# Kernel tuning notes

Measured on AMD Instinct MI355X. Metric: run time of the kernel, lower is better.

## Reference

```python
import jax, jax.numpy as jnp
import numpy as np

N = 100000        # total nodes across the batch of graphs
E = 1600000       # directed edges (avg degree 16)
B = 64            # number of graphs
IN_C = 4
HID = 128


def gcn_conv(x, W, b, src, dst, n):
    """PyG GCNConv: add self-loops, symmetric deg normalization, scatter-add."""
    h = x @ W                                   # [n, out]
    loop = jnp.arange(n)
    s = jnp.concatenate([src, loop])            # [E+n] sources (with self-loops)
    d = jnp.concatenate([dst, loop])            # [E+n] targets
    deg = jax.ops.segment_sum(jnp.ones_like(s, dtype=h.dtype), d, num_segments=n)
    dinv = jnp.where(deg > 0, jax.lax.rsqrt(deg), 0.0)
    norm = dinv[s] * dinv[d]                    # [E+n]
    out = jax.ops.segment_sum(h[s] * norm[:, None], d, num_segments=n)
    return out + b


def setup_inputs() -> dict:
    key = jax.random.key(0)
    k1, k2, k3, k4, k5, k6, k7 = jax.random.split(key, 7)
    x = jax.random.normal(k1, (N, IN_C), dtype=jnp.float32)
    edge_index = jax.random.randint(k2, (2, E), 0, N, dtype=jnp.int64)
    batch = jnp.sort(jax.random.randint(k3, (N,), 0, B, dtype=jnp.int64))
    W1 = jax.random.normal(k4, (IN_C, HID), dtype=jnp.float32) / np.sqrt(IN_C)
    b1 = jnp.zeros((HID,), dtype=jnp.float32)
    W2 = jax.random.normal(k5, (HID, HID), dtype=jnp.float32) / np.sqrt(HID)
    b2 = jnp.zeros((HID,), dtype=jnp.float32)
    return {"x": x, "edge_index": edge_index, "batch": batch,
            "W1": W1, "b1": b1, "W2": W2, "b2": b2}


def reference(x, edge_index, batch, W1, b1, W2, b2):
    src, dst = edge_index[0], edge_index[1]
    n = x.shape[0]
    h = jax.nn.relu(gcn_conv(x, W1, b1, src, dst, n))
    h = jax.nn.relu(gcn_conv(h, W2, b2, src, dst, n))
    # global_mean_pool: scatter-mean by graph id
    s = jax.ops.segment_sum(h, batch, num_segments=B)                       # [B, HID]
    cnt = jax.ops.segment_sum(jnp.ones((n,), h.dtype), batch, num_segments=B)
    return s / jnp.maximum(cnt, 1.0)[:, None]
```

## Files before the change

kernel.cpp:

```cpp
#include <hip/hip_runtime.h>

#define TPB 256
#define HID 128
#define IN_C 4
#define SLOT_C 32
#define NB 512
#define EPT 8
#define ECAP 4096
#define OVF_CAP 131072

typedef __attribute__((ext_vector_type(8))) short bf16x8;
typedef __attribute__((ext_vector_type(4))) float f32x4;

union FragU { uint4 u; bf16x8 b; };

__device__ __forceinline__ unsigned f2bf(float f) {
    unsigned u = __float_as_uint(f);
    return (u + 0x7fffu + ((u >> 16) & 1u)) >> 16;
}
__device__ __forceinline__ float bf_lo(unsigned u) { return __uint_as_float(u << 16); }
__device__ __forceinline__ float bf_hi(unsigned u) { return __uint_as_float(u & 0xffff0000u); }

__global__ void k_prep(int* cursor, float* out, int n, int outsz,
                       const float* __restrict__ W2, unsigned short* w2f,
                       const int* __restrict__ batch, float* rcnt, int bg,
                       int* ovf_cnt, int* pcur) {
    int nbA = (n + TPB - 1) / TPB;
    int b = blockIdx.x;
    if (b < nbA) {
        int i = b * TPB + threadIdx.x;
        if (i < n) cursor[i] = 0;
        if (i < outsz) out[i] = 0.0f;
    } else if (b < nbA + 64) {
        int i = (b - nbA) * TPB + threadIdx.x;
        if (i < HID * HID) {
            int j = i & 7, frag = i >> 3;
            int lane = frag & 63, blk = frag >> 6;
            int kk = blk >> 3, nt = blk & 7;
            int quad = lane >> 4, nloc = lane & 15;
            int k = kk * 32 + quad * 8 + j;
            int c = nt * 16 + nloc;
            w2f[i] = (unsigned short)f2bf(W2[k * HID + c]);
        }
    } else {
        int g = threadIdx.x;
        if (g == 0) *ovf_cnt = 0;
        for (int z = g; z < NB; z += TPB) pcur[z] = 0;
        if (g < bg) {
            int lo0 = 0, hi0 = n;
            while (lo0 < hi0) { int m = (lo0 + hi0) >> 1; if (batch[m] < g) lo0 = m + 1; else hi0 = m; }
            int lo1 = lo0, hi1 = n;
            while (lo1 < hi1) { int m = (lo1 + hi1) >> 1; if (batch[m] < g + 1) lo1 = m + 1; else hi1 = m; }
            int c = lo1 - lo0;
            rcnt[g] = 1.0f / (float)(c > 1 ? c : 1);
        }
    }
}

__global__ __launch_bounds__(256) void k_part(
        const int* __restrict__ src, const int* __restrict__ dst,
        int2* elist, int* pcur, int e, int n) {
    __shared__ int lcnt[2][NB];
    __shared__ int lbase[NB];
    int t = threadIdx.x;
    int c = (t >> 5) & 1;
    for (int z = t; z < NB; z += 256) { lcnt[0][z] = 0; lcnt[1][z] = 0; }
    __syncthreads();

    int base_i = blockIdx.x * (256 * EPT);
    int s[EPT], d[EPT], pr[EPT];
#pragma unroll
    for (int k = 0; k < EPT; k++) {
        int i = base_i + k * 256 + t;
        if (i < e) {
            s[k] = src[i];
            d[k] = dst[i];
            int p = (int)(((long long)d[k] * NB) / n);
            int r = atomicAdd(&lcnt[c][p], 1);
            pr[k] = p | (r << 9);
        } else {
            pr[k] = -1;
        }
    }
    __syncthreads();

    for (int z = t; z < NB; z += 256) {
        int tot = lcnt[0][z] + lcnt[1][z];
        lbase[z] = tot ? atomicAdd(&pcur[z], tot) : 0;
    }
    __syncthreads();

#pragma unroll
    for (int k = 0; k < EPT; k++) {
        if (pr[k] >= 0) {
            int p = pr[k] & (NB - 1);
            int r = pr[k] >> 9;
            int idx = lbase[p] + (c ? lcnt[0][p] : 0) + r;
            if (idx < ECAP)
                elist[(size_t)p * ECAP + idx] = make_int2(s[k], d[k]);
        }
    }
}

__global__ __launch_bounds__(256) void k_build(
        const int2* __restrict__ elist, const int* __restrict__ pcur,
        int* cursor, float* dinv, int* slots, int* ovf, int* ovf_cnt, int n) {
    __shared__ int lcur[512];
    int p = blockIdx.x;
    int t = threadIdx.x;
    int nlo = (int)(((long long)p * n + NB - 1) / NB);
    int nhi = (int)(((long long)(p + 1) * n + NB - 1) / NB);
    int nn = nhi - nlo;
    for (int z = t; z < nn; z += 256) lcur[z] = 0;
    __syncthreads();

    int ne = pcur[p];
    if (ne > ECAP) ne = ECAP;
    for (int j = t; j < ne; j += 256) {
        int2 ed = elist[(size_t)p * ECAP + j];
        int pos = atomicAdd(&lcur[ed.y - nlo], 1);
        if (pos < SLOT_C) {
            slots[ed.y * SLOT_C + pos] = ed.x;
        } else {
            int o = atomicAdd(ovf_cnt, 1);
            if (o < OVF_CAP) {
                ovf[2 * o] = ed.x;
                ovf[2 * o + 1] = ed.y;
            }
        }
    }
    __syncthreads();
    for (int z = t; z < nn; z += 256) {
        int dg = lcur[z];
        cursor[nlo + z] = dg;
        dinv[nlo + z] = rsqrtf((float)dg + 1.0f);
    }
}

__global__ __launch_bounds__(256) void k_g1f1(
        const int* __restrict__ cursor, const int* __restrict__ slots,
        const int* __restrict__ ovf, const int* __restrict__ ovf_cnt,
        const float* __restrict__ dinv, const float* __restrict__ x,
        const float* __restrict__ W1, const float* __restrict__ b1,
        unsigned* f1p, int n) {
    __shared__ float xs[256 * 5];
    int t = threadIdx.x;
    int v0 = blockIdx.x * 256;

    int v = v0 + t;
    if (v < n) {
        float dv = dinv[v];
        const float4* x4 = (const float4*)x;
        float4 xv = x4[v];
        float sl = dv * dv;
        float4 A = make_float4(sl * xv.x, sl * xv.y, sl * xv.z, sl * xv.w);
        float4 B = make_float4(0.f, 0.f, 0.f, 0.f);
        float4 C = make_float4(0.f, 0.f, 0.f, 0.f);
        float4 D = make_float4(0.f, 0.f, 0.f, 0.f);
        int deg = cursor[v];
        int m = deg < SLOT_C ? deg : SLOT_C;
        const int* sb = slots + v * SLOT_C;
        int e = 0;
        for (; e + 4 <= m; e += 4) {
            int s0 = sb[e], s1 = sb[e + 1], s2 = sb[e + 2], s3 = sb[e + 3];
            float n0 = dinv[s0] * dv, n1 = dinv[s1] * dv;
            float n2 = dinv[s2] * dv, n3 = dinv[s3] * dv;
            float4 r0 = x4[s0], r1 = x4[s1], r2 = x4[s2], r3 = x4[s3];
            A.x = fmaf(n0, r0.x, A.x); A.y = fmaf(n0, r0.y, A.y);
            A.z = fmaf(n0, r0.z, A.z); A.w = fmaf(n0, r0.w, A.w);
            B.x = fmaf(n1, r1.x, B.x); B.y = fmaf(n1, r1.y, B.y);
            B.z = fmaf(n1, r1.z, B.z); B.w = fmaf(n1, r1.w, B.w);
            C.x = fmaf(n2, r2.x, C.x); C.y = fmaf(n2, r2.y, C.y);
            C.z = fmaf(n2, r2.z, C.z); C.w = fmaf(n2, r2.w, C.w);
            D.x = fmaf(n3, r3.x, D.x); D.y = fmaf(n3, r3.y, D.y);
            D.z = fmaf(n3, r3.z, D.z); D.w = fmaf(n3, r3.w, D.w);
        }
        for (; e < m; e++) {
            int s = sb[e];
            float nm = dinv[s] * dv;
            float4 r = x4[s];
            A.x = fmaf(nm, r.x, A.x); A.y = fmaf(nm, r.y, A.y);
            A.z = fmaf(nm, r.z, A.z); A.w = fmaf(nm, r.w, A.w);
        }
        if (deg > SLOT_C) {
            int oc = *ovf_cnt;
            for (int k = 0; k < oc; k++) {
                if (ovf[2 * k + 1] == v) {
                    int s = ovf[2 * k];
                    float nm = dinv[s] * dv;
                    float4 r = x4[s];
                    A.x = fmaf(nm, r.x, A.x); A.y = fmaf(nm, r.y, A.y);
                    A.z = fmaf(nm, r.z, A.z); A.w = fmaf(nm, r.w, A.w);
                }
            }
        }
        xs[t * 5 + 0] = (A.x + B.x) + (C.x + D.x);
        xs[t * 5 + 1] = (A.y + B.y) + (C.y + D.y);
        xs[t * 5 + 2] = (A.z + B.z) + (C.z + D.z);
        xs[t * 5 + 3] = (A.w + B.w) + (C.w + D.w);
    }
    __syncthreads();

    int cp = t & 63;
    int c0 = cp * 2, c1 = c0 + 1;
    float w00 = W1[c0],           w01 = W1[c1];
    float w10 = W1[HID + c0],     w11 = W1[HID + c1];
    float w20 = W1[2 * HID + c0], w21 = W1[2 * HID + c1];
    float w30 = W1[3 * HID + c0], w31 = W1[3 * HID + c1];
    float bb0 = b1[c0],           bb1 = b1[c1];
    int g = t >> 6;
    for (int iter = 0; iter < 64; iter++) {
        int node = iter * 4 + g;
        int vv = v0 + node;
        if (vv >= n) break;
        float x0 = xs[node * 5 + 0], x1 = xs[node * 5 + 1];
        float x2 = xs[node * 5 + 2], x3 = xs[node * 5 + 3];
        float s0 = fmaf(x0, w00, fmaf(x1, w10, fmaf(x2, w20, fmaf(x3, w30, bb0))));
        float s1 = fmaf(x0, w01, fmaf(x1, w11, fmaf(x2, w21, fmaf(x3, w31, bb1))));
        s0 = s0 > 0.0f ? s0 : 0.0f;
        s1 = s1 > 0.0f ? s1 : 0.0f;
        f1p[(size_t)vv * 64 + cp] = f2bf(s0) | (f2bf(s1) << 16);
    }
}

__global__ __launch_bounds__(128) void k_gather2(
        const int* __restrict__ cursor, const int* __restrict__ slots,
        const int* __restrict__ ovf, const int* __restrict__ ovf_cnt,
        const float* __restrict__ dinv, const unsigned* __restrict__ f1p,
        unsigned* acc2b, int n) {
    int wv = threadIdx.x >> 6;
    int ln = threadIdx.x & 63;
    int h  = ln >> 5;
    int q  = ln & 31;
    int v = blockIdx.x * 2 + wv;
    if (v >= n) return;
    float dv = dinv[v];
    const uint2* F = (const uint2*)f1p;

    uint2 us = F[(size_t)v * 32 + q];
    float sl = (h == 0) ? dv * dv : 0.0f;
    float A[4] = { sl * bf_lo(us.x), sl * bf_hi(us.x),
                   sl * bf_lo(us.y), sl * bf_hi(us.y) };
    float B[4] = {0.f, 0.f, 0.f, 0.f};
    float C[4] = {0.f, 0.f, 0.f, 0.f};
    float D[4] = {0.f, 0.f, 0.f, 0.f};

    int deg = cursor[v];
    int m = deg < SLOT_C ? deg : SLOT_C;
    const int* sb = slots + v * SLOT_C;
    int e = 0;
    for (; e + 8 <= m; e += 8) {
        int sA = sb[e + h];
        int sB = sb[e + 2 + h];
        int sC = sb[e + 4 + h];
        int sD = sb[e + 6 + h];
        float nA = dinv[sA] * dv, nB = dinv[sB] * dv;
        float nC = dinv[sC] * dv, nD = dinv[sD] * dv;
        uint2 uA = F[(size_t)sA * 32 + q];
        uint2 uB = F[(size_t)sB * 32 + q];
        uint2 uC = F[(size_t)sC * 32 + q];
        uint2 uD = F[(size_t)sD * 32 + q];
        A[0] = fmaf(nA, bf_lo(uA.x), A[0]); A[1] = fmaf(nA, bf_hi(uA.x), A[1]);
        A[2] = fmaf(nA, bf_lo(uA.y), A[2]); A[3] = fmaf(nA, bf_hi(uA.y), A[3]);
        B[0] = fmaf(nB, bf_lo(uB.x), B[0]); B[1] = fmaf(nB, bf_hi(uB.x), B[1]);
        B[2] = fmaf(nB, bf_lo(uB.y), B[2]); B[3] = fmaf(nB, bf_hi(uB.y), B[3]);
        C[0] = fmaf(nC, bf_lo(uC.x), C[0]); C[1] = fmaf(nC, bf_hi(uC.x), C[1]);
        C[2] = fmaf(nC, bf_lo(uC.y), C[2]); C[3] = fmaf(nC, bf_hi(uC.y), C[3]);
        D[0] = fmaf(nD, bf_lo(uD.x), D[0]); D[1] = fmaf(nD, bf_hi(uD.x), D[1]);
        D[2] = fmaf(nD, bf_lo(uD.y), D[2]); D[3] = fmaf(nD, bf_hi(uD.y), D[3]);
    }
    for (; e + 2 <= m; e += 2) {
        int s = sb[e + h];
        float nm = dinv[s] * dv;
        uint2 u = F[(size_t)s * 32 + q];
        A[0] = fmaf(nm, bf_lo(u.x), A[0]); A[1] = fmaf(nm, bf_hi(u.x), A[1]);
        A[2] = fmaf(nm, bf_lo(u.y), A[2]); A[3] = fmaf(nm, bf_hi(u.y), A[3]);
    }
    if (e < m) {
        int s = sb[e];
        float nm = (h == 0) ? dinv[s] * dv : 0.0f;
        uint2 u = F[(size_t)s * 32 + q];
        A[0] = fmaf(nm, bf_lo(u.x), A[0]); A[1] = fmaf(nm, bf_hi(u.x), A[1]);
        A[2] = fmaf(nm, bf_lo(u.y), A[2]); A[3] = fmaf(nm, bf_hi(u.y), A[3]);
    }
    if (deg > SLOT_C) {
        int oc = *ovf_cnt;
        for (int k = 0; k < oc; k++) {
            if (ovf[2 * k + 1] == v && h == 0) {
                int s = ovf[2 * k];
                float nm = dinv[s] * dv;
                uint2 u = F[(size_t)s * 32 + q];
                A[0] = fmaf(nm, bf_lo(u.x), A[0]); A[1] = fmaf(nm, bf_hi(u.x), A[1]);
                A[2] = fmaf(nm, bf_lo(u.y), A[2]); A[3] = fmaf(nm, bf_hi(u.y), A[3]);
            }
        }
    }

    float o0 = (A[0] + B[0]) + (C[0] + D[0]);
    float o1 = (A[1] + B[1]) + (C[1] + D[1]);
    float o2 = (A[2] + B[2]) + (C[2] + D[2]);
    float o3 = (A[3] + B[3]) + (C[3] + D[3]);
    o0 += __shfl_xor(o0, 32, 64);
    o1 += __shfl_xor(o1, 32, 64);
    o2 += __shfl_xor(o2, 32, 64);
    o3 += __shfl_xor(o3, 32, 64);
    if (h == 0) {
        uint2 w;
        w.x = f2bf(o0) | (f2bf(o1) << 16);
        w.y = f2bf(o2) | (f2bf(o3) << 16);
        ((uint2*)acc2b)[(size_t)v * 32 + q] = w;
    }
}

__global__ __launch_bounds__(256) void k_mm2_pool(
        const unsigned* __restrict__ acc2b, const unsigned short* __restrict__ w2f,
        const float* __restrict__ b2, const int* __restrict__ batch,
        const float* __restrict__ rcnt, float* out, int n) {
    __shared__ int bch[64];
    int t = threadIdx.x;
    int w = t >> 6, lane = t & 63;
    int quad = lane >> 4, nloc = lane & 15;
    int v0 = blockIdx.x * 64;
    if (t < 64) {
        int v = v0 + t;
        bch[t] = (v < n) ? batch[v] : -1;
    }
    __syncthreads();

    int va = v0 + w * 16 + nloc;
    if (va >= n) va = n - 1;

    const uint4* A4 = (const uint4*)acc2b;
    const uint4* B4 = (const uint4*)w2f;

    f32x4 acc[8];
#pragma unroll
    for (int nt = 0; nt < 8; nt++) acc[nt] = (f32x4){0.f, 0.f, 0.f, 0.f};

#pragma unroll
    for (int kk = 0; kk < 4; kk++) {
        FragU af;
        af.u = A4[(size_t)va * 16 + kk * 4 + quad];
#pragma unroll
        for (int nt = 0; nt < 8; nt++) {
            FragU bf;
            bf.u = B4[(kk * 8 + nt) * 64 + lane];
            acc[nt] = __builtin_amdgcn_mfma_f32_16x16x32_bf16(af.b, bf.b, acc[nt], 0, 0, 0);
        }
    }

    int b0 = bch[w * 16], b15 = bch[w * 16 + 15];
    if (b0 == b15 && b0 >= 0) {
        float rc = rcnt[b0];
#pragma unroll
        for (int nt = 0; nt < 8; nt++) {
            float bias = b2[nt * 16 + nloc];
            float s = 0.f;
#pragma unroll
            for (int reg = 0; reg < 4; reg++) {
                float f = acc[nt][reg] + bias;
                s += f > 0.f ? f : 0.f;
            }
            s += __shfl_xor(s, 16, 64);
            s += __shfl_xor(s, 32, 64);
            if (lane < 16) atomicAdd(&out[b0 * HID + nt * 16 + lane], s * rc);
        }
    } else {
#pragma unroll
        for (int nt = 0; nt < 8; nt++) {
            float bias = b2[nt * 16 + nloc];
            int cur = -1; float run = 0.f;
#pragma unroll
            for (int reg = 0; reg < 4; reg++) {
                int b = bch[w * 16 + quad * 4 + reg];
                if (b < 0) continue;
                float f = acc[nt][reg] + bias;
                f = f > 0.f ? f : 0.f;
                if (b != cur) {
                    if (cur >= 0) atomicAdd(&out[cur * HID + nt * 16 + nloc], run * rcnt[cur]);
                    run = 0.f; cur = b;
                }
                run += f;
            }
            if (cur >= 0) atomicAdd(&out[cur * HID + nt * 16 + nloc], run * rcnt[cur]);
        }
    }
}

extern "C" void kernel_launch(void* const* d_in, const int* in_sizes, int n_in,
                              void* d_out, int out_size, void* d_ws, size_t ws_size,
                              hipStream_t stream) {
    const float* x   = (const float*)d_in[0];
    const int* ei    = (const int*)d_in[1];
    const int* batch = (const int*)d_in[2];
    const float* W1  = (const float*)d_in[3];
    const float* b1  = (const float*)d_in[4];
    const float* W2  = (const float*)d_in[5];
    const float* b2  = (const float*)d_in[6];
    float* out = (float*)d_out;

    int n  = in_sizes[0] / IN_C;
    int e  = in_sizes[1] / 2;
    int bg = out_size / HID;
    const int* src = ei;
    const int* dst = ei + e;

    size_t off_b = 0;
    char* base = (char*)d_ws;
    auto carve = [&](size_t bytes) -> void* {
        void* p = base + off_b;
        off_b += (bytes + 255) & ~(size_t)255;
        return p;
    };
    int*            cursor  = (int*)carve((size_t)n * 4);
    int*            slots   = (int*)carve((size_t)n * SLOT_C * 4);
    int*            ovf     = (int*)carve((size_t)OVF_CAP * 2 * 4);
    int*            ovf_cnt = (int*)carve(256);
    int*            pcur    = (int*)carve((size_t)NB * 4);
    int2*           elist   = (int2*)carve((size_t)NB * ECAP * 8);
    float*          dinv    = (float*)carve((size_t)n * 4);
    unsigned*       f1p     = (unsigned*)carve((size_t)n * 64 * 4);
    unsigned*       acc2b   = (unsigned*)carve((size_t)n * 64 * 4);
    unsigned short* w2f     = (unsigned short*)carve((size_t)HID * HID * 2);
    float*          rcnt    = (float*)carve((size_t)bg * 4);
    (void)ws_size;

    int gN = (n + TPB - 1) / TPB;
    int gP = (e + 256 * EPT - 1) / (256 * EPT);

    k_prep<<<gN + 64 + 1, TPB, 0, stream>>>(cursor, out, n, out_size, W2, w2f,
                                            batch, rcnt, bg, ovf_cnt, pcur);
    k_part<<<gP, TPB, 0, stream>>>(src, dst, elist, pcur, e, n);
    k_build<<<NB, TPB, 0, stream>>>(elist, pcur, cursor, dinv, slots, ovf, ovf_cnt, n);
    k_g1f1<<<gN, TPB, 0, stream>>>(cursor, slots, ovf, ovf_cnt, dinv, x, W1, b1, f1p, n);
    k_gather2<<<(n + 1) / 2, 128, 0, stream>>>(cursor, slots, ovf, ovf_cnt, dinv, f1p, acc2b, n);
    k_mm2_pool<<<(n + 63) / 64, 256, 0, stream>>>(acc2b, w2f, b2, batch, rcnt, out, n);
}
```

Baseline: 248.0 us.

## Fuse layer-2 gather with MFMA matmul and pooling via shared-memory rows

Merges the layer-2 neighbor gather kernel into the matmul+pool kernel. Each 256-thread block gathers 64 node rows, with each wave handling 16 nodes in turn, and stages the aggregated bf16 rows in LDS, padded to 68 words per row. It then feeds them to the MFMA tile directly. This removes the acc2b global round trip (write then read of n*128 bf16) and one kernel launch. The cost is less parallelism in the gather: 64 nodes per block processed serially per wave instead of 2 nodes per 128-thread block, which may hurt latency hiding for the random gathers.

Result: slower. 285.5 us (+15.1%).

```diff
diff --git a/kernel.cpp b/kernel.cpp
--- a/kernel.cpp
+++ b/kernel.cpp
@@ -223,114 +223,112 @@
     }
 }
 
-__global__ __launch_bounds__(128) void k_gather2(
+__global__ __launch_bounds__(256) void k_g2mm(
         const int* __restrict__ cursor, const int* __restrict__ slots,
         const int* __restrict__ ovf, const int* __restrict__ ovf_cnt,
         const float* __restrict__ dinv, const unsigned* __restrict__ f1p,
-        unsigned* acc2b, int n) {
-    int wv = threadIdx.x >> 6;
-    int ln = threadIdx.x & 63;
-    int h  = ln >> 5;
-    int q  = ln & 31;
-    int v = blockIdx.x * 2 + wv;
-    if (v >= n) return;
-    float dv = dinv[v];
-    const uint2* F = (const uint2*)f1p;
-
-    uint2 us = F[(size_t)v * 32 + q];
-    float sl = (h == 0) ? dv * dv : 0.0f;
-    float A[4] = { sl * bf_lo(us.x), sl * bf_hi(us.x),
-                   sl * bf_lo(us.y), sl * bf_hi(us.y) };
-    float B[4] = {0.f, 0.f, 0.f, 0.f};
-    float C[4] = {0.f, 0.f, 0.f, 0.f};
-    float D[4] = {0.f, 0.f, 0.f, 0.f};
-
-    int deg = cursor[v];
-    int m = deg < SLOT_C ? deg : SLOT_C;
-    const int* sb = slots + v * SLOT_C;
-    int e = 0;
-    for (; e + 8 <= m; e += 8) {
-        int sA = sb[e + h];
-        int sB = sb[e + 2 + h];
-        int sC = sb[e + 4 + h];
-        int sD = sb[e + 6 + h];
-        float nA = dinv[sA] * dv, nB = dinv[sB] * dv;
-        float nC = dinv[sC] * dv, nD = dinv[sD] * dv;
-        uint2 uA = F[(size_t)sA * 32 + q];
-        uint2 uB = F[(size_t)sB * 32 + q];
-        uint2 uC = F[(size_t)sC * 32 + q];
-        uint2 uD = F[(size_t)sD * 32 + q];
-        A[0] = fmaf(nA, bf_lo(uA.x), A[0]); A[1] = fmaf(nA, bf_hi(uA.x), A[1]);
-        A[2] = fmaf(nA, bf_lo(uA.y), A[2]); A[3] = fmaf(nA, bf_hi(uA.y), A[3]);
-        B[0] = fmaf(nB, bf_lo(uB.x), B[0]); B[1] = fmaf(nB, bf_hi(uB.x), B[1]);
-        B[2] = fmaf(nB, bf_lo(uB.y), B[2]); B[3] = fmaf(nB, bf_hi(uB.y), B[3]);
-        C[0] = fmaf(nC, bf_lo(uC.x), C[0]); C[1] = fmaf(nC, bf_hi(uC.x), C[1]);
-        C[2] = fmaf(nC, bf_lo(uC.y), C[2]); C[3] = fmaf(nC, bf_hi(uC.y), C[3]);
-        D[0] = fmaf(nD, bf_lo(uD.x), D[0]); D[1] = fmaf(nD, bf_hi(uD.x), D[1]);
-        D[2] = fmaf(nD, bf_lo(uD.y), D[2]); D[3] = fmaf(nD, bf_hi(uD.y), D[3]);
-    }
-    for (; e + 2 <= m; e += 2) {
-        int s = sb[e + h];
-        float nm = dinv[s] * dv;
-        uint2 u = F[(size_t)s * 32 + q];
-        A[0] = fmaf(nm, bf_lo(u.x), A[0]); A[1] = fmaf(nm, bf_hi(u.x), A[1]);
-        A[2] = fmaf(nm, bf_lo(u.y), A[2]); A[3] = fmaf(nm, bf_hi(u.y), A[3]);
-    }
-    if (e < m) {
-        int s = sb[e];
-        float nm = (h == 0) ? dinv[s] * dv : 0.0f;
-        uint2 u = F[(size_t)s * 32 + q];
-        A[0] = fmaf(nm, bf_lo(u.x), A[0]); A[1] = fmaf(nm, bf_hi(u.x), A[1]);
-        A[2] = fmaf(nm, bf_lo(u.y), A[2]); A[3] = fmaf(nm, bf_hi(u.y), A[3]);
-    }
-    if (deg > SLOT_C) {
-        int oc = *ovf_cnt;
-        for (int k = 0; k < oc; k++) {
-            if (ovf[2 * k + 1] == v && h == 0) {
-                int s = ovf[2 * k];
-                float nm = dinv[s] * dv;
-                uint2 u = F[(size_t)s * 32 + q];
-                A[0] = fmaf(nm, bf_lo(u.x), A[0]); A[1] = fmaf(nm, bf_hi(u.x), A[1]);
-                A[2] = fmaf(nm, bf_lo(u.y), A[2]); A[3] = fmaf(nm, bf_hi(u.y), A[3]);
-            }
-        }
-    }
-
-    float o0 = (A[0] + B[0]) + (C[0] + D[0]);
-    float o1 = (A[1] + B[1]) + (C[1] + D[1]);
-    float o2 = (A[2] + B[2]) + (C[2] + D[2]);
-    float o3 = (A[3] + B[3]) + (C[3] + D[3]);
-    o0 += __shfl_xor(o0, 32, 64);
-    o1 += __shfl_xor(o1, 32, 64);
-    o2 += __shfl_xor(o2, 32, 64);
-    o3 += __shfl_xor(o3, 32, 64);
-    if (h == 0) {
-        uint2 w;
-        w.x = f2bf(o0) | (f2bf(o1) << 16);
-        w.y = f2bf(o2) | (f2bf(o3) << 16);
-        ((uint2*)acc2b)[(size_t)v * 32 + q] = w;
-    }
-}
-
-__global__ __launch_bounds__(256) void k_mm2_pool(
-        const unsigned* __restrict__ acc2b, const unsigned short* __restrict__ w2f,
-        const float* __restrict__ b2, const int* __restrict__ batch,
-        const float* __restrict__ rcnt, float* out, int n) {
+        const unsigned short* __restrict__ w2f, const float* __restrict__ b2,
+        const int* __restrict__ batch, const float* __restrict__ rcnt,
+        float* out, int n) {
+    __shared__ unsigned arow[64][68];
     __shared__ int bch[64];
     int t = threadIdx.x;
-    int w = t >> 6, lane = t & 63;
-    int quad = lane >> 4, nloc = lane & 15;
+    int w = t >> 6, ln = t & 63;
     int v0 = blockIdx.x * 64;
     if (t < 64) {
         int v = v0 + t;
         bch[t] = (v < n) ? batch[v] : -1;
     }
-    __syncthreads();
-
-    int va = v0 + w * 16 + nloc;
-    if (va >= n) va = n - 1;
-
-    const uint4* A4 = (const uint4*)acc2b;
+    if (v0 + 64 > n) {
+        for (int z = t; z < 64 * 68; z += 256) ((unsigned*)arow)[z] = 0;
+    }
+    __syncthreads();
+
+    int h = ln >> 5;
+    int q = ln & 31;
+    const uint2* F = (const uint2*)f1p;
+    for (int nd = 0; nd < 16; nd++) {
+        int row = w * 16 + nd;
+        int v = v0 + row;
+        if (v >= n) break;
+        float dv = dinv[v];
+
+        uint2 us = F[(size_t)v * 32 + q];
+        float sl = (h == 0) ? dv * dv : 0.0f;
+        float A[4] = { sl * bf_lo(us.x), sl * bf_hi(us.x),
+                       sl * bf_lo(us.y), sl * bf_hi(us.y) };
+        float B[4] = {0.f, 0.f, 0.f, 0.f};
+        float C[4] = {0.f, 0.f, 0.f, 0.f};
+        float D[4] = {0.f, 0.f, 0.f, 0.f};
+
+        int deg = cursor[v];
+        int m = deg < SLOT_C ? deg : SLOT_C;
+        const int* sb = slots + v * SLOT_C;
+        int e = 0;
+        for (; e + 8 <= m; e += 8) {
+            int sA = sb[e + h];
+            int sB = sb[e + 2 + h];
+            int sC = sb[e + 4 + h];
+            int sD = sb[e + 6 + h];
+            float nA = dinv[sA] * dv, nB = dinv[sB] * dv;
+            float nC = dinv[sC] * dv, nD = dinv[sD] * dv;
+            uint2 uA = F[(size_t)sA * 32 + q];
+            uint2 uB = F[(size_t)sB * 32 + q];
+            uint2 uC = F[(size_t)sC * 32 + q];
+            uint2 uD = F[(size_t)sD * 32 + q];
+            A[0] = fmaf(nA, bf_lo(uA.x), A[0]); A[1] = fmaf(nA, bf_hi(uA.x), A[1]);
+            A[2] = fmaf(nA, bf_lo(uA.y), A[2]); A[3] = fmaf(nA, bf_hi(uA.y), A[3]);
+            B[0] = fmaf(nB, bf_lo(uB.x), B[0]); B[1] = fmaf(nB, bf_hi(uB.x), B[1]);
+            B[2] = fmaf(nB, bf_lo(uB.y), B[2]); B[3] = fmaf(nB, bf_hi(uB.y), B[3]);
+            C[0] = fmaf(nC, bf_lo(uC.x), C[0]); C[1] = fmaf(nC, bf_hi(uC.x), C[1]);
+            C[2] = fmaf(nC, bf_lo(uC.y), C[2]); C[3] = fmaf(nC, bf_hi(uC.y), C[3]);
+            D[0] = fmaf(nD, bf_lo(uD.x), D[0]); D[1] = fmaf(nD, bf_hi(uD.x), D[1]);
+            D[2] = fmaf(nD, bf_lo(uD.y), D[2]); D[3] = fmaf(nD, bf_hi(uD.y), D[3]);
+        }
+        for (; e + 2 <= m; e += 2) {
+            int s = sb[e + h];
+            float nm = dinv[s] * dv;
+            uint2 u = F[(size_t)s * 32 + q];
+            A[0] = fmaf(nm, bf_lo(u.x), A[0]); A[1] = fmaf(nm, bf_hi(u.x), A[1]);
+            A[2] = fmaf(nm, bf_lo(u.y), A[2]); A[3] = fmaf(nm, bf_hi(u.y), A[3]);
+        }
+        if (e < m) {
+            int s = sb[e];
+            float nm = (h == 0) ? dinv[s] * dv : 0.0f;
+            uint2 u = F[(size_t)s * 32 + q];
+            A[0] = fmaf(nm, bf_lo(u.x), A[0]); A[1] = fmaf(nm, bf_hi(u.x), A[1]);
+            A[2] = fmaf(nm, bf_lo(u.y), A[2]); A[3] = fmaf(nm, bf_hi(u.y), A[3]);
+        }
+        if (deg > SLOT_C) {
+            int oc = *ovf_cnt;
+            for (int k = 0; k < oc; k++) {
+                if (ovf[2 * k + 1] == v && h == 0) {
+                    int s = ovf[2 * k];
+                    float nm = dinv[s] * dv;
+                    uint2 u = F[(size_t)s * 32 + q];
+                    A[0] = fmaf(nm, bf_lo(u.x), A[0]); A[1] = fmaf(nm, bf_hi(u.x), A[1]);
+                    A[2] = fmaf(nm, bf_lo(u.y), A[2]); A[3] = fmaf(nm, bf_hi(u.y), A[3]);
+                }
+            }
+        }
+
+        float o0 = (A[0] + B[0]) + (C[0] + D[0]);
+        float o1 = (A[1] + B[1]) + (C[1] + D[1]);
+        float o2 = (A[2] + B[2]) + (C[2] + D[2]);
+        float o3 = (A[3] + B[3]) + (C[3] + D[3]);
+        o0 += __shfl_xor(o0, 32, 64);
+        o1 += __shfl_xor(o1, 32, 64);
+        o2 += __shfl_xor(o2, 32, 64);
+        o3 += __shfl_xor(o3, 32, 64);
+        if (h == 0) {
+            arow[row][2 * q]     = f2bf(o0) | (f2bf(o1) << 16);
+            arow[row][2 * q + 1] = f2bf(o2) | (f2bf(o3) << 16);
+        }
+    }
+    __syncthreads();
+
+    int lane = ln;
+    int quad = lane >> 4, nloc = lane & 15;
     const uint4* B4 = (const uint4*)w2f;
 
     f32x4 acc[8];
@@ -340,7 +338,7 @@
 #pragma unroll
     for (int kk = 0; kk < 4; kk++) {
         FragU af;
-        af.u = A4[(size_t)va * 16 + kk * 4 + quad];
+        af.u = *(const uint4*)&arow[w * 16 + nloc][(kk * 4 + quad) * 4];
 #pragma unroll
         for (int nt = 0; nt < 8; nt++) {
             FragU bf;
@@ -420,7 +418,6 @@
     int2*           elist   = (int2*)carve((size_t)NB * ECAP * 8);
     float*          dinv    = (float*)carve((size_t)n * 4);
     unsigned*       f1p     = (unsigned*)carve((size_t)n * 64 * 4);
-    unsigned*       acc2b   = (unsigned*)carve((size_t)n * 64 * 4);
     unsigned short* w2f     = (unsigned short*)carve((size_t)HID * HID * 2);
     float*          rcnt    = (float*)carve((size_t)bg * 4);
     (void)ws_size;
@@ -433,6 +430,6 @@
     k_part<<<gP, TPB, 0, stream>>>(src, dst, elist, pcur, e, n);
     k_build<<<NB, TPB, 0, stream>>>(elist, pcur, cursor, dinv, slots, ovf, ovf_cnt, n);
     k_g1f1<<<gN, TPB, 0, stream>>>(cursor, slots, ovf, ovf_cnt, dinv, x, W1, b1, f1p, n);
-    k_gather2<<<(n + 1) / 2, 128, 0, stream>>>(cursor, slots, ovf, ovf_cnt, dinv, f1p, acc2b, n);
-    k_mm2_pool<<<(n + 63) / 64, 256, 0, stream>>>(acc2b, w2f, b2, batch, rcnt, out, n);
-}
+    k_g2mm<<<(n + 63) / 64, 256, 0, stream>>>(cursor, slots, ovf, ovf_cnt, dinv, f1p,
+                                              w2f, b2, batch, rcnt, out, n);
+}
```
